# Kernel optimization log

Measured on AMD Instinct MI355X. Metric: run time of the kernel, lower is better.

## Reference

```python
import jax, jax.numpy as jnp
import numpy as np

N = 8192
IN_DIM = 256
OUT_DIM = 256


def setup_inputs() -> dict:
    key = jax.random.key(0)
    k1, k2, k3, k4 = jax.random.split(key, 4)
    x = jax.random.normal(k1, (N, IN_DIM), dtype=jnp.float32)
    adj = jax.random.uniform(k2, (N, N), dtype=jnp.float32)
    # nn.Linear(in_dim, out_dim): weight [out,in], bias [out]. Store W as [in,out].
    bound = 1.0 / np.sqrt(IN_DIM)
    W = jax.random.uniform(k3, (IN_DIM, OUT_DIM), dtype=jnp.float32, minval=-bound, maxval=bound)
    b = jax.random.uniform(k4, (OUT_DIM,), dtype=jnp.float32, minval=-bound, maxval=bound)
    return {"x": x, "adj": adj, "W": W, "b": b}


def reference(x, adj, W, b):
    # ReLU( D^{-1/2} (A + I) D^{-1/2} X W + b )
    # A_hat = adj + I; degree = A_hat.sum(axis=1)
    n = adj.shape[0]
    A_hat = adj + jnp.eye(n, dtype=adj.dtype)
    degree = A_hat.sum(axis=1)
    d_inv_sqrt = degree ** -0.5  # [N]
    # D^{-1/2} @ A_hat @ D^{-1/2} == row-scale then col-scale (no NxN diag matmuls)
    A_norm = A_hat * d_inv_sqrt[:, None] * d_inv_sqrt[None, :]
    out = A_norm @ x          # [N, in_dim]
    out = out @ W + b         # [N, out_dim]
    return jax.nn.relu(out)
```

## Files before the change

### kernel.cpp

```cpp
#include <hip/hip_runtime.h>


typedef __attribute__((ext_vector_type(8))) short short8;
typedef __attribute__((ext_vector_type(4))) float floatx4;

#define GLDS16(g, l) __builtin_amdgcn_global_load_lds(\
    (const __attribute__((address_space(1))) void*)(g), \
    (__attribute__((address_space(3))) void*)(l), 16, 0, 0)

__device__ __forceinline__ unsigned short f2b(float f) {
  unsigned int x = __builtin_bit_cast(unsigned int, f);
  unsigned int r = (x + 0x7fffu + ((x >> 16) & 1u)) >> 16;
  return (unsigned short)r;
}

__global__ __launch_bounds__(512) void k_deg(
    const float* __restrict__ adj, unsigned short* __restrict__ adjb,
    float* __restrict__ degree4) {
  __shared__ float part[8][64];
  const int t = threadIdx.x, l = t & 63, w = t >> 6;
  const int mb = blockIdx.x >> 2, sk = blockIdx.x & 3;
  const int m0 = mb * 64;
  const float* src = adj + (size_t)(m0 + l) * 8192 + sk * 2048;
  unsigned short* dstBase = adjb + ((size_t)(mb * 4 + sk) * 16384 + l) * 8;
  float rs = 0.f;
  for (int i = w * 8; i < w * 8 + 8; ++i) {
    const float* s = src + i * 32;
#pragma unroll
    for (int q = 0; q < 4; ++q) {
      float4 v0 = *(const float4*)(s + q * 8);
      float4 v1 = *(const float4*)(s + q * 8 + 4);
      short8 u;
      u[0] = f2b(v0.x); u[1] = f2b(v0.y); u[2] = f2b(v0.z); u[3] = f2b(v0.w);
      u[4] = f2b(v1.x); u[5] = f2b(v1.y); u[6] = f2b(v1.z); u[7] = f2b(v1.w);
      *(short8*)(dstBase + (size_t)(i * 4 + q) * 512) = u;
      rs += ((v0.x + v0.y) + (v0.z + v0.w)) + ((v1.x + v1.y) + (v1.z + v1.w));
    }
  }
  part[w][l] = rs;
  __syncthreads();
  if (t < 64) {
    float s = 0.f;
#pragma unroll
    for (int ww = 0; ww < 8; ++ww) s += part[ww][t];
    degree4[sk * 8192 + m0 + t] = s;
  }
}

__global__ __launch_bounds__(256) void k_xw(
    const float* __restrict__ X, const float* __restrict__ W,
    const float* __restrict__ bias, const float* __restrict__ degree4,
    float* __restrict__ Zd, unsigned short* __restrict__ Zsb,
    float* __restrict__ sinv) {
  __shared__ unsigned short ldsT[256 * 20];
  const int t = threadIdx.x, l = t & 63, w = t >> 6;
  const int m0 = blockIdx.x * 16;
  const int r0 = w * 4;
  const int n0 = l * 4;
  const float* Xp = X + (size_t)(m0 + r0) * 256;
  float acc[4][4] = {};
#pragma unroll 2
  for (int k = 0; k < 256; k += 4) {
    float4 wv[4];
#pragma unroll
    for (int j = 0; j < 4; ++j) wv[j] = *(const float4*)(W + (size_t)(k + j) * 256 + n0);
#pragma unroll
    for (int r = 0; r < 4; ++r) {
      float4 xv = *(const float4*)(Xp + r * 256 + k);
      const float xs[4] = {xv.x, xv.y, xv.z, xv.w};
#pragma unroll
      for (int j = 0; j < 4; ++j) {
        acc[r][0] += xs[j] * wv[j].x;
        acc[r][1] += xs[j] * wv[j].y;
        acc[r][2] += xs[j] * wv[j].z;
        acc[r][3] += xs[j] * wv[j].w;
      }
    }
  }
  const float4 bv = *(const float4*)(bias + n0);
#pragma unroll
  for (int r = 0; r < 4; ++r) {
    const int row = m0 + r0 + r;
    const float deg = degree4[row] + degree4[8192 + row]
                    + degree4[16384 + row] + degree4[24576 + row];
    const float sr = rsqrtf(deg + 1.0f);
    if (l == 0) sinv[row] = sr;
    float4 zd;
    zd.x = sr * sr * acc[r][0] + bv.x;
    zd.y = sr * sr * acc[r][1] + bv.y;
    zd.z = sr * sr * acc[r][2] + bv.z;
    zd.w = sr * sr * acc[r][3] + bv.w;
    *(float4*)(Zd + (size_t)row * 256 + n0) = zd;
#pragma unroll
    for (int n = 0; n < 4; ++n)
      ldsT[(size_t)(n0 + n) * 20 + (r0 + r)] = f2b(sr * acc[r][n]);
  }
  __syncthreads();
  const int kt = m0 >> 6, kcb = (m0 >> 3) & 7;
#pragma unroll
  for (int c = 0; c < 2; ++c) {
    const unsigned short* p = ldsT + (size_t)t * 20 + c * 8;
    short8 vv;
#pragma unroll
    for (int j = 0; j < 8; ++j) vv[j] = p[j];
    *(short8*)(Zsb + ((size_t)kt * 2048 + (kcb + c) * 256 + t) * 8) = vv;
  }
}

__global__ __launch_bounds__(512) void k_main(
    const unsigned short* __restrict__ adjb, const unsigned short* __restrict__ Zsb,
    float* __restrict__ P) {
  __shared__ __align__(16) char lds[2][20608];
  const int t = threadIdx.x, l = t & 63, w = t >> 6;
  const int quad = l >> 4, nl = l & 15;
  const int bm = blockIdx.x >> 2, sk = blockIdx.x & 3;
  const int m0 = bm * 64;
  const int wm = w & 1, wn = w >> 1;
  const unsigned short* aBase = adjb + (size_t)(bm * 4 + sk) * 131072;
  const unsigned short* bBase = Zsb + (size_t)sk * 524288;
  floatx4 acc[2][4] = {};

  if (t < 256)
    GLDS16(aBase + (size_t)t * 8, lds[0] + (t >> 6) * 1040 + (t & 63) * 16);
#pragma unroll
  for (int q = 0; q < 2; ++q) {
    const int sl = q * 512 + t;
    GLDS16(bBase + (size_t)sl * 8, lds[0] + 4224 + sl * 16);
  }
  __syncthreads();

  for (int i = 0; i < 64; ++i) {
    const int cur = i & 1, nxt = cur ^ 1;
    const int ib = i < 63 ? i + 1 : 63;
    if (t < 256)
      GLDS16(aBase + ((size_t)ib * 256 + t) * 8,
             lds[nxt] + (t >> 6) * 1040 + (t & 63) * 16);
#pragma unroll
    for (int q = 0; q < 2; ++q) {
      const int sl = q * 512 + t;
      GLDS16(bBase + ((size_t)ib * 1024 + sl) * 8, lds[nxt] + 4224 + sl * 16);
    }
    const char* rA = lds[cur];
    const char* rB = lds[cur] + 4224;
    short8 af[2], bf[4];
    af[0] = *(const short8*)(rA + quad * 1040 + (wm * 32 + nl) * 16);
    af[1] = *(const short8*)(rA + quad * 1040 + (wm * 32 + 16 + nl) * 16);
#pragma unroll
    for (int nf = 0; nf < 4; ++nf) {
      const int col = wn * 64 + nf * 16 + nl;
      bf[nf] = *(const short8*)(rB + ((size_t)quad * 256 + col) * 16);
    }
#pragma unroll
    for (int mi = 0; mi < 2; ++mi)
#pragma unroll
      for (int nf = 0; nf < 4; ++nf)
        acc[mi][nf] = __builtin_amdgcn_mfma_f32_16x16x32_bf16(af[mi], bf[nf], acc[mi][nf], 0, 0, 0);
    __syncthreads();
  }

  float* Pk = P + (size_t)sk * 8192 * 256;
#pragma unroll
  for (int mi = 0; mi < 2; ++mi)
#pragma unroll
    for (int nf = 0; nf < 4; ++nf)
#pragma unroll
      for (int r = 0; r < 4; ++r) {
        const int row = m0 + wm * 32 + mi * 16 + quad * 4 + r;
        const int col = wn * 64 + nf * 16 + nl;
        Pk[(size_t)row * 256 + col] = acc[mi][nf][r];
      }
}

__global__ __launch_bounds__(256) void k_fin(
    const float* __restrict__ P, const float* __restrict__ Zd,
    const float* __restrict__ sinv, float* __restrict__ out) {
  const int i = blockIdx.x * 256 + threadIdx.x;
  const int row = i >> 6;
  const float sr = sinv[row];
  const size_t stride = (size_t)8192 * 256;
  float4 p0 = *(const float4*)(P + (size_t)i * 4);
  float4 p1 = *(const float4*)(P + stride + (size_t)i * 4);
  float4 p2 = *(const float4*)(P + 2 * stride + (size_t)i * 4);
  float4 p3 = *(const float4*)(P + 3 * stride + (size_t)i * 4);
  const float4 zd = *(const float4*)(Zd + (size_t)i * 4);
  float4 v;
  v.x = sr * ((p0.x + p1.x) + (p2.x + p3.x)) + zd.x;
  v.y = sr * ((p0.y + p1.y) + (p2.y + p3.y)) + zd.y;
  v.z = sr * ((p0.z + p1.z) + (p2.z + p3.z)) + zd.z;
  v.w = sr * ((p0.w + p1.w) + (p2.w + p3.w)) + zd.w;
  v.x = v.x > 0.f ? v.x : 0.f;
  v.y = v.y > 0.f ? v.y : 0.f;
  v.z = v.z > 0.f ? v.z : 0.f;
  v.w = v.w > 0.f ? v.w : 0.f;
  *(float4*)(out + (size_t)i * 4) = v;
}

extern "C" void kernel_launch(void* const* d_in, const int* in_sizes, int n_in,
                              void* d_out, int out_size, void* d_ws, size_t ws_size,
                              hipStream_t stream) {
  const float* X    = (const float*)d_in[0];
  const float* adj  = (const float*)d_in[1];
  const float* W    = (const float*)d_in[2];
  const float* bias = (const float*)d_in[3];
  float* out = (float*)d_out;
  char* ws = (char*)d_ws;

  float* degree4       = (float*)(ws);
  float* sinv          = (float*)(ws + (256 << 10));
  float* Zd            = (float*)(ws + (1 << 20));
  unsigned short* Zsb  = (unsigned short*)(ws + (9 << 20));
  float* P             = (float*)(ws + (13 << 20));
  unsigned short* adjb = (unsigned short*)(ws + (45 << 20));

  hipLaunchKernelGGL(k_deg,  dim3(512),  dim3(512), 0, stream, adj, adjb, degree4);
  hipLaunchKernelGGL(k_xw,   dim3(512),  dim3(256), 0, stream, X, W, bias, degree4, Zd, Zsb, sinv);
  hipLaunchKernelGGL(k_main, dim3(512),  dim3(512), 0, stream, adjb, Zsb, P);
  hipLaunchKernelGGL(k_fin,  dim3(2048), dim3(256), 0, stream, P, Zd, sinv, out);
}
```

Baseline: 529.4 us.

## Coalesce adjacency conversion via LDS transpose and enlarge main GEMM tiles

The degree/convert kernel now reads adjacency rows with lanes spread along each row, so global loads are coalesced. It transposes the bf16 tiles through a swizzled LDS buffer before writing them out, and reduces row sums with wave shuffles into eight partial-degree slices. The main bf16 GEMM moves to 128x128 output tiles with K=64 per stage, 256 threads and two blocks per CU, which raises operand reuse per LDS load and halves the loop trips. The cost is more LDS per block and more accumulator registers, which may limit occupancy.

```diff
diff --git a/kernel.cpp b/kernel.cpp
--- a/kernel.cpp
+++ b/kernel.cpp
@@ -16,40 +16,54 @@
 
 __global__ __launch_bounds__(512) void k_deg(
     const float* __restrict__ adj, unsigned short* __restrict__ adjb,
-    float* __restrict__ degree4) {
-  __shared__ float part[8][64];
-  const int t = threadIdx.x, l = t & 63, w = t >> 6;
-  const int mb = blockIdx.x >> 2, sk = blockIdx.x & 3;
-  const int m0 = mb * 64;
-  const float* src = adj + (size_t)(m0 + l) * 8192 + sk * 2048;
-  unsigned short* dstBase = adjb + ((size_t)(mb * 4 + sk) * 16384 + l) * 8;
-  float rs = 0.f;
-  for (int i = w * 8; i < w * 8 + 8; ++i) {
-    const float* s = src + i * 32;
-#pragma unroll
-    for (int q = 0; q < 4; ++q) {
-      float4 v0 = *(const float4*)(s + q * 8);
-      float4 v1 = *(const float4*)(s + q * 8 + 4);
+    float* __restrict__ degree8) {
+  __shared__ __align__(16) char xlds[65536];
+  const int t = threadIdx.x, g = t >> 5, c = t & 31;
+  const int mb2 = blockIdx.x >> 3, sk = (blockIdx.x >> 1) & 3, h = blockIdx.x & 1;
+  const float* src = adj + (size_t)mb2 * 128 * 8192 + sk * 2048 + h * 1024;
+  unsigned short* dstP = adjb
+      + ((size_t)(mb2 * 4 + sk) * 32768 + (size_t)h * 16384) * 8;
+  float rs[8] = {};
+#pragma unroll
+  for (int s = 0; s < 4; ++s) {
+#pragma unroll
+    for (int rr = 0; rr < 8; ++rr) {
+      const int row = rr * 16 + g;
+      const float* p = src + (size_t)row * 8192 + s * 256 + c * 8;
+      float4 v0 = *(const float4*)(p);
+      float4 v1 = *(const float4*)(p + 4);
+      rs[rr] += ((v0.x + v0.y) + (v0.z + v0.w)) + ((v1.x + v1.y) + (v1.z + v1.w));
       short8 u;
       u[0] = f2b(v0.x); u[1] = f2b(v0.y); u[2] = f2b(v0.z); u[3] = f2b(v0.w);
       u[4] = f2b(v1.x); u[5] = f2b(v1.y); u[6] = f2b(v1.z); u[7] = f2b(v1.w);
-      *(short8*)(dstBase + (size_t)(i * 4 + q) * 512) = u;
-      rs += ((v0.x + v0.y) + (v0.z + v0.w)) + ((v1.x + v1.y) + (v1.z + v1.w));
-    }
-  }
-  part[w][l] = rs;
-  __syncthreads();
-  if (t < 64) {
-    float s = 0.f;
-#pragma unroll
-    for (int ww = 0; ww < 8; ++ww) s += part[ww][t];
-    degree4[sk * 8192 + m0 + t] = s;
+      *(short8*)(xlds + c * 2048 + ((row ^ (c & 7)) * 16)) = u;
+    }
+    __syncthreads();
+    unsigned short* dst = dstP + (size_t)s * 4096 * 8;
+#pragma unroll
+    for (int j = 0; j < 8; ++j) {
+      const int lu = j * 512 + t;
+      const int U = lu >> 7, R = lu & 127;
+      short8 u = *(const short8*)(xlds + U * 2048 + ((R ^ (U & 7)) * 16));
+      *(short8*)(dst + (size_t)lu * 8) = u;
+    }
+    __syncthreads();
+  }
+#pragma unroll
+  for (int rr = 0; rr < 8; ++rr) {
+#pragma unroll
+    for (int o = 16; o > 0; o >>= 1) rs[rr] += __shfl_down(rs[rr], o, 32);
+  }
+  if (c == 0) {
+    float* dp = degree8 + (size_t)(sk * 2 + h) * 8192 + mb2 * 128;
+#pragma unroll
+    for (int rr = 0; rr < 8; ++rr) dp[rr * 16 + g] = rs[rr];
   }
 }
 
 __global__ __launch_bounds__(256) void k_xw(
     const float* __restrict__ X, const float* __restrict__ W,
-    const float* __restrict__ bias, const float* __restrict__ degree4,
+    const float* __restrict__ bias, const float* __restrict__ degree8,
     float* __restrict__ Zd, unsigned short* __restrict__ Zsb,
     float* __restrict__ sinv) {
   __shared__ unsigned short ldsT[256 * 20];
@@ -81,8 +95,9 @@
 #pragma unroll
   for (int r = 0; r < 4; ++r) {
     const int row = m0 + r0 + r;
-    const float deg = degree4[row] + degree4[8192 + row]
-                    + degree4[16384 + row] + degree4[24576 + row];
+    float deg = 0.f;
+#pragma unroll
+    for (int p = 0; p < 8; ++p) deg += degree8[(size_t)p * 8192 + row];
     const float sr = rsqrtf(deg + 1.0f);
     if (l == 0) sinv[row] = sr;
     float4 zd;
@@ -107,65 +122,67 @@
   }
 }
 
-__global__ __launch_bounds__(512) void k_main(
+__global__ __launch_bounds__(256, 2) void k_main(
     const unsigned short* __restrict__ adjb, const unsigned short* __restrict__ Zsb,
     float* __restrict__ P) {
-  __shared__ __align__(16) char lds[2][20608];
+  __shared__ __align__(16) char lds[2][33024];
   const int t = threadIdx.x, l = t & 63, w = t >> 6;
   const int quad = l >> 4, nl = l & 15;
-  const int bm = blockIdx.x >> 2, sk = blockIdx.x & 3;
-  const int m0 = bm * 64;
+  const int bm2 = blockIdx.x >> 3, bn = (blockIdx.x >> 2) & 1, sk = blockIdx.x & 3;
   const int wm = w & 1, wn = w >> 1;
-  const unsigned short* aBase = adjb + (size_t)(bm * 4 + sk) * 131072;
-  const unsigned short* bBase = Zsb + (size_t)sk * 524288;
-  floatx4 acc[2][4] = {};
-
-  if (t < 256)
-    GLDS16(aBase + (size_t)t * 8, lds[0] + (t >> 6) * 1040 + (t & 63) * 16);
-#pragma unroll
-  for (int q = 0; q < 2; ++q) {
-    const int sl = q * 512 + t;
-    GLDS16(bBase + (size_t)sl * 8, lds[0] + 4224 + sl * 16);
+  const unsigned short* aBase = adjb + (size_t)(bm2 * 4 + sk) * 32768 * 8;
+  const unsigned short* bBase = Zsb + ((size_t)sk * 32 * 2048 + bn * 128) * 8;
+  floatx4 acc[4][4] = {};
+
+#pragma unroll
+  for (int p = 0; p < 4; ++p) {
+    const int j = p * 256 + t;
+    const int q = j >> 7, rr = j & 127;
+    GLDS16(aBase + (size_t)j * 8, lds[0] + q * 2064 + rr * 16);
+    GLDS16(bBase + (size_t)(q * 256 + rr) * 8, lds[0] + 16512 + q * 2064 + rr * 16);
   }
   __syncthreads();
 
-  for (int i = 0; i < 64; ++i) {
+  for (int i = 0; i < 32; ++i) {
     const int cur = i & 1, nxt = cur ^ 1;
-    const int ib = i < 63 ? i + 1 : 63;
-    if (t < 256)
-      GLDS16(aBase + ((size_t)ib * 256 + t) * 8,
-             lds[nxt] + (t >> 6) * 1040 + (t & 63) * 16);
-#pragma unroll
-    for (int q = 0; q < 2; ++q) {
-      const int sl = q * 512 + t;
-      GLDS16(bBase + ((size_t)ib * 1024 + sl) * 8, lds[nxt] + 4224 + sl * 16);
+    const int ib = i < 31 ? i + 1 : 31;
+#pragma unroll
+    for (int p = 0; p < 4; ++p) {
+      const int j = p * 256 + t;
+      const int q = j >> 7, rr = j & 127;
+      GLDS16(aBase + ((size_t)ib * 1024 + j) * 8, lds[nxt] + q * 2064 + rr * 16);
+      GLDS16(bBase + ((size_t)ib * 2048 + q * 256 + rr) * 8,
+             lds[nxt] + 16512 + q * 2064 + rr * 16);
     }
     const char* rA = lds[cur];
-    const char* rB = lds[cur] + 4224;
-    short8 af[2], bf[4];
-    af[0] = *(const short8*)(rA + quad * 1040 + (wm * 32 + nl) * 16);
-    af[1] = *(const short8*)(rA + quad * 1040 + (wm * 32 + 16 + nl) * 16);
-#pragma unroll
-    for (int nf = 0; nf < 4; ++nf) {
-      const int col = wn * 64 + nf * 16 + nl;
-      bf[nf] = *(const short8*)(rB + ((size_t)quad * 256 + col) * 16);
-    }
-#pragma unroll
-    for (int mi = 0; mi < 2; ++mi)
+    const char* rB = lds[cur] + 16512;
+#pragma unroll
+    for (int kk = 0; kk < 2; ++kk) {
+      const int qq = kk * 4 + quad;
+      short8 af[4], bf[4];
+#pragma unroll
+      for (int mi = 0; mi < 4; ++mi)
+        af[mi] = *(const short8*)(rA + qq * 2064 + (wm * 64 + mi * 16 + nl) * 16);
 #pragma unroll
       for (int nf = 0; nf < 4; ++nf)
-        acc[mi][nf] = __builtin_amdgcn_mfma_f32_16x16x32_bf16(af[mi], bf[nf], acc[mi][nf], 0, 0, 0);
+        bf[nf] = *(const short8*)(rB + qq * 2064 + (wn * 64 + nf * 16 + nl) * 16);
+#pragma unroll
+      for (int mi = 0; mi < 4; ++mi)
+#pragma unroll
+        for (int nf = 0; nf < 4; ++nf)
+          acc[mi][nf] = __builtin_amdgcn_mfma_f32_16x16x32_bf16(af[mi], bf[nf], acc[mi][nf], 0, 0, 0);
+    }
     __syncthreads();
   }
 
-  float* Pk = P + (size_t)sk * 8192 * 256;
-#pragma unroll
-  for (int mi = 0; mi < 2; ++mi)
+  float* Pk = P + (size_t)sk * 8192 * 256 + (size_t)bn * 128;
+#pragma unroll
+  for (int mi = 0; mi < 4; ++mi)
 #pragma unroll
     for (int nf = 0; nf < 4; ++nf)
 #pragma unroll
       for (int r = 0; r < 4; ++r) {
-        const int row = m0 + wm * 32 + mi * 16 + quad * 4 + r;
+        const int row = bm2 * 128 + wm * 64 + mi * 16 + quad * 4 + r;
         const int col = wn * 64 + nf * 16 + nl;
         Pk[(size_t)row * 256 + col] = acc[mi][nf][r];
       }
@@ -205,15 +222,15 @@
   float* out = (float*)d_out;
   char* ws = (char*)d_ws;
 
-  float* degree4       = (float*)(ws);
-  float* sinv          = (float*)(ws + (256 << 10));
+  float* degree8       = (float*)(ws);
+  float* sinv          = (float*)(ws + (512 << 10));
   float* Zd            = (float*)(ws + (1 << 20));
   unsigned short* Zsb  = (unsigned short*)(ws + (9 << 20));
   float* P             = (float*)(ws + (13 << 20));
   unsigned short* adjb = (unsigned short*)(ws + (45 << 20));
 
-  hipLaunchKernelGGL(k_deg,  dim3(512),  dim3(512), 0, stream, adj, adjb, degree4);
-  hipLaunchKernelGGL(k_xw,   dim3(512),  dim3(256), 0, stream, X, W, bias, degree4, Zd, Zsb, sinv);
-  hipLaunchKernelGGL(k_main, dim3(512),  dim3(512), 0, stream, adjb, Zsb, P);
+  hipLaunchKernelGGL(k_deg,  dim3(512),  dim3(512), 0, stream, adj, adjb, degree8);
+  hipLaunchKernelGGL(k_xw,   dim3(512),  dim3(256), 0, stream, X, W, bias, degree8, Zd, Zsb, sinv);
+  hipLaunchKernelGGL(k_main, dim3(512),  dim3(256), 0, stream, adjb, Zsb, P);
   hipLaunchKernelGGL(k_fin,  dim3(2048), dim3(256), 0, stream, P, Zd, sinv, out);
 }
```

Result: no change. 525.2 us (-0.8%).
